# Performance work log

Measured on AMD Instinct MI355X. Metric: run time of the kernel, lower is better.

The kernel has to match this reference:

```python
import jax, jax.numpy as jnp
import numpy as np

BEAM = 10; MAX_LEN = 32; PAD = 1; BOS = 2; EOS = 3
NEG = jnp.float32(-1e30)


def lstm_cell(x, h, c, Wih, Whh, bih, bhh):
    # PyTorch LSTMCell gate order: i, f, g, o
    gates = x @ Wih.T + bih + h @ Whh.T + bhh
    i, f, g, o = jnp.split(gates, 4, axis=-1)
    c2 = jax.nn.sigmoid(f) * c + jax.nn.sigmoid(i) * jnp.tanh(g)
    h2 = jax.nn.sigmoid(o) * jnp.tanh(c2)
    return h2, c2


def setup_inputs() -> dict:
    key = jax.random.key(0)
    ks = jax.random.split(key, 14)
    G, P, E, H, S = 1000, 50000, 500, 500, 32
    s = lambda k, shape: jax.random.normal(k, shape, jnp.float32) * 0.05
    return {
        "g_seq": jax.random.randint(ks[0], (S, 1), 0, G),
        "enc_emb": s(ks[1], (G, E)),
        "enc_Wih": s(ks[2], (4 * H, E)), "enc_Whh": s(ks[3], (4 * H, H)),
        "enc_bih": s(ks[4], (4 * H,)), "enc_bhh": s(ks[5], (4 * H,)),
        "dec_emb": s(ks[6], (P, E)),
        "dec_Wih": s(ks[7], (4 * H, E)), "dec_Whh": s(ks[8], (4 * H, H)),
        "dec_bih": s(ks[9], (4 * H,)), "dec_bhh": s(ks[10], (4 * H,)),
        "attn_W": s(ks[11], (H, 2 * H)),
        "out_W": s(ks[12], (P, H)),
        "out_b": s(ks[13], (P,)),
    }


def reference(g_seq, enc_emb, enc_Wih, enc_Whh, enc_bih, enc_bhh,
              dec_emb, dec_Wih, dec_Whh, dec_bih, dec_bhh,
              attn_W, out_W, out_b):
    S = g_seq.shape[0]
    H = enc_Whh.shape[1]
    P = out_W.shape[0]

    # ---- encoder: unidirectional LSTMCell over seq, batch = 1 ----
    e_seq = enc_emb[g_seq[:, 0]]  # (S, E)
    def enc_step(carry, e):
        h, c = carry
        h, c = lstm_cell(e[None, :], h, c, enc_Wih, enc_Whh, enc_bih, enc_bhh)
        return (h, c), h[0]
    h0 = jnp.zeros((1, H), jnp.float32)
    (h, c), outs = jax.lax.scan(enc_step, (h0, h0), e_seq)  # outs: (S, H)

    # expand encoder state / context to beam
    context = jnp.broadcast_to(outs[None, :, :], (BEAM, S, H))
    h = jnp.broadcast_to(h, (BEAM, H))
    c = jnp.broadcast_to(c, (BEAM, H))
    scores = jnp.zeros((BEAM,), jnp.float32)
    tokens = jnp.full((BEAM,), PAD, jnp.int32).at[0].set(BOS)
    row0 = (jnp.arange(BEAM)[:, None] == 0)  # first-step mask: only beam 0 valid

    # ---- beam-search decode loop (run full max_len; early-eos break omitted,
    #      see notes: with eos=3 it only changes output when eos tops beam 0) ----
    def dec_step(carry, t):
        h, c, scores, tokens = carry
        e = dec_emb[tokens]                                   # (BEAM, E)
        h2, c2 = lstm_cell(e, h, c, dec_Wih, dec_Whh, dec_bih, dec_bhh)
        # dot attention
        attn = jax.nn.softmax(jnp.einsum('bsh,bh->bs', context, h2), axis=1)
        wctx = jnp.einsum('bs,bsh->bh', attn, context)
        o = jnp.tanh(jnp.concatenate([h2, wctx], axis=1) @ attn_W.T)
        logp = jax.nn.log_softmax(o @ out_W.T + out_b, axis=1)  # (BEAM, P)
        # first step: only beam 0 participates (original uses workd_lk[0])
        beam_lk = jnp.where(t == 0,
                            jnp.where(row0, logp, NEG),
                            logp + scores[:, None])
        best, idx = jax.lax.top_k(beam_lk.reshape(-1), BEAM)
        prev_k = idx // P
        next_y = idx - prev_k * P
        return (h2[prev_k], c2[prev_k], best, next_y), (prev_k, next_y)

    (_, _, scores, _), (prevKs, nextYs) = jax.lax.scan(
        dec_step, (h, c, scores, tokens), jnp.arange(MAX_LEN))

    # ---- hypothesis traceback, vectorized over beams ----
    def tb_step(k, t):
        tok = nextYs[t][k]
        return prevKs[t][k], tok
    _, toks = jax.lax.scan(tb_step, jnp.arange(BEAM), jnp.arange(MAX_LEN - 1, -1, -1))
    hyps = toks[::-1].T  # (BEAM, MAX_LEN)
    return hyps
```

## Files before the change

### kernel.cpp

```cpp
#include <hip/hip_runtime.h>
#include <hip/hip_cooperative_groups.h>
#include <math.h>

namespace cg = cooperative_groups;

#define BEAM   10
#define MAXLEN 32
#define SLEN   32
#define HD     500
#define ED     500
#define G4     2000
#define PV     50000
#define NEGF   (-1e30f)

#define GRID   256
#define NW     1024

#define NCHUNK 25
#define CHSZ   2000
#define CANDN  (NCHUNK * BEAM * BEAM)

#define OFF_X      0
#define OFF_CBUF   64000
#define OFF_GBUF   65000
#define OFF_CTX    69000
#define OFF_DH     85000
#define OFF_DC     90000
#define OFF_DG     95000
#define OFF_H2     115000
#define OFF_C2     120000
#define OFF_O      130000
#define OFF_SCD    135000
#define OFF_TOK    135020
#define OFF_PREVK  135040
#define OFF_NEXTY  135360
#define OFF_PARTD  136000
#define OFF_CAND   152000
#define OFF_LOG    160000
#define OFF_OWT    660000
#define NEED_T_BYTES ((size_t)(OFF_OWT + (size_t)HD * PV) * 4)

typedef unsigned long long u64;

__device__ __forceinline__ float sigf(float x) { return 1.f / (1.f + expf(-x)); }

__device__ __forceinline__ unsigned fkey(float f) {
    unsigned u = __float_as_uint(f);
    return (u & 0x80000000u) ? ~u : (u | 0x80000000u);
}
__device__ __forceinline__ float unfkey(unsigned k) {
    unsigned u = (k & 0x80000000u) ? (k & 0x7fffffffu) : ~k;
    return __uint_as_float(u);
}

__global__ void k_prep(const int* __restrict__ g_seq, const float* __restrict__ enc_emb,
                       const float* __restrict__ Wih, const float* __restrict__ bih,
                       const float* __restrict__ bhh, float* __restrict__ X,
                       float* __restrict__ cbuf0) {
    if (blockIdx.x == 0) {
        for (int j = threadIdx.x; j < HD; j += 256) cbuf0[j] = 0.f;
    }
    int wv = (blockIdx.x * blockDim.x + threadIdx.x) >> 6;
    int lane = threadIdx.x & 63;
    if (wv >= SLEN * G4) return;
    int t = wv / G4, r = wv - t * G4;
    const float* emb = enc_emb + (size_t)g_seq[t] * ED;
    const float* w = Wih + (size_t)r * ED;
    float acc = 0.f;
    for (int ki = 0; ki < 8; ki++) { int k = ki * 64 + lane; if (k < ED) acc += emb[k] * w[k]; }
    for (int o = 32; o; o >>= 1) acc += __shfl_down(acc, o);
    if (lane == 0) X[t * G4 + r] = acc + bih[r] + bhh[r];
}

__global__ void k_transpose4(const float* __restrict__ outW, float* __restrict__ outW4) {
    __shared__ float t_lds[64][65];
    int tid = threadIdx.x;
    int pbase = blockIdx.x * 64, kbase = blockIdx.y * 64;
    for (int e = 0; e < 16; e++) {
        int idx = e * 256 + tid; int pl = idx >> 6, kl = idx & 63;
        int pp = pbase + pl, kk = kbase + kl;
        t_lds[pl][kl] = (pp < PV && kk < HD) ? outW[(size_t)pp * HD + kk] : 0.f;
    }
    __syncthreads();
    for (int e = 0; e < 4; e++) {
        int idx = e * 256 + tid;
        int pl = idx & 63, kb = idx >> 6;
        int pp = pbase + pl;
        int kglob = kbase + kb * 4;
        if (pp < PV && kglob < HD) {
            float4 v;
            v.x = t_lds[pl][kb * 4 + 0];
            v.y = t_lds[pl][kb * 4 + 1];
            v.z = t_lds[pl][kb * 4 + 2];
            v.w = t_lds[pl][kb * 4 + 3];
            *(float4*)(outW4 + ((size_t)(kbase / 4 + kb) * PV + pp) * 4) = v;
        }
    }
}

struct MegaA {
    const float* encWhh; const float* X;
    float* gbuf; float* cbuf; float* ctx;
    const float* decEmb; const float* decWih; const float* decWhh;
    const float* decBih; const float* decBhh; const float* attnW;
    const float* outW4; const float* outW; const float* outB;
    float* dh; float* dc; float* dg; float* h2w; float* c2w; float* ow;
    float* logits; double* sc; double* part;
    int* tok; int* prevK; int* nextY; u64* cand; int* outTok;
    int bigws; int npart;
};

struct TopkSm { u64 wred[4]; u64 win; };
struct MergeSm {
    double wredd[4];
    double lse[BEAM];
    double scl[BEAM];
    double bwv[4];
    unsigned bwf[4];
    unsigned winf;
    int pk[BEAM]; int ny[BEAM];
    double val[BEAM];
};

__global__ __launch_bounds__(256) void k_mega(MegaA A) {
    __shared__ __align__(16) char smem_raw[43584];
    float* smf = (float*)smem_raw;
    cg::grid_group grid = cg::this_grid();
    const int tid = threadIdx.x, bid = blockIdx.x;
    const int wv = tid >> 6, lane = tid & 63;
    const int gw = bid * 4 + wv;

    for (int t = 0; t <= SLEN; ++t) {
        const float* gprev = A.gbuf + ((t + 1) & 1) * G4;
        float*       gcur  = A.gbuf + (t & 1) * G4;
        const float* cprev = A.cbuf + ((t + 1) & 1) * HD;
        float*       ccur  = A.cbuf + (t & 1) * HD;
        bool par = (t < SLEN) || (bid == 0);
        if (par) {
            float* h_lds = smf;
            if (t > 0) {
                for (int j = tid; j < HD; j += 256) {
                    float gi = gprev[j], gf = gprev[HD + j], gg = gprev[2 * HD + j], go = gprev[3 * HD + j];
                    float c = sigf(gf) * cprev[j] + sigf(gi) * tanhf(gg);
                    float h = sigf(go) * tanhf(c);
                    h_lds[j] = h;
                    if (bid == 0) {
                        ccur[j] = c;
                        A.ctx[(t - 1) * HD + j] = h;
                        if (t == SLEN) {
                            for (int b = 0; b < BEAM; b++) { A.dh[b * HD + j] = h; A.dc[b * HD + j] = c; }
                        }
                    }
                }
            } else {
                for (int j = tid; j < HD; j += 256) h_lds[j] = 0.f;
            }
            if (t == SLEN && bid == 0 && tid == 0) {
                for (int b = 0; b < BEAM; b++) A.sc[b] = 0.0;
                A.tok[0] = 2; for (int b = 1; b < BEAM; b++) A.tok[b] = 1;
            }
            __syncthreads();
            if (t < SLEN) {
                for (int r = gw; r < G4; r += NW) {
                    const float* w = A.encWhh + (size_t)r * HD;
                    float acc = 0.f;
                    for (int ki = 0; ki < 8; ki++) { int k = ki * 64 + lane; if (k < HD) acc += h_lds[k] * w[k]; }
                    for (int o = 32; o; o >>= 1) acc += __shfl_down(acc, o);
                    if (lane == 0) gcur[r] = A.X[t * G4 + r] + acc;
                }
            }
        }
        grid.sync();
    }

    for (int t = 0; t < MAXLEN; ++t) {
        {
            float* e_lds = smf;
            float* h_lds = smf + BEAM * ED;
            for (int idx = tid; idx < BEAM * ED; idx += 256) {
                int b = idx / ED, k = idx - b * ED;
                e_lds[idx] = A.decEmb[(size_t)A.tok[b] * ED + k];
                h_lds[idx] = A.dh[idx];
            }
            __syncthreads();
            for (int r = gw; r < G4; r += NW) {
                const float* wi = A.decWih + (size_t)r * ED;
                const float* wh = A.decWhh + (size_t)r * HD;
                float acc[BEAM];
#pragma unroll
                for (int b = 0; b < BEAM; b++) acc[b] = 0.f;
                for (int ki = 0; ki < 8; ki++) {
                    int k = ki * 64 + lane;
                    if (k < ED) {
                        float w = wi[k];
#pragma unroll
                        for (int b = 0; b < BEAM; b++) acc[b] += w * e_lds[b * ED + k];
                    }
                }
                for (int ki = 0; ki < 8; ki++) {
                    int k = ki * 64 + lane;
                    if (k < HD) {
                        float w = wh[k];
#pragma unroll
                        for (int b = 0; b < BEAM; b++) acc[b] += w * h_lds[b * HD + k];
                    }
                }
#pragma unroll
                for (int b = 0; b < BEAM; b++) {
                    float v = acc[b];
                    for (int o = 32; o; o >>= 1) v += __shfl_down(v, o);
                    acc[b] = v;
                }
                if (lane == 0) {
                    float bb = A.decBih[r] + A.decBhh[r];
#pragma unroll
                    for (int b = 0; b < BEAM; b++) A.dg[b * G4 + r] = acc[b] + bb;
                }
            }
        }
        grid.sync();

        if (bid < 125) {
            float* h2_lds   = smf;
            float* wctx_lds = smf + 5000;
            float* s_lds    = smf + 10000;
            float* a_lds    = smf + 10320;
            for (int idx = tid; idx < BEAM * HD; idx += 256) {
                int b = idx / HD, j = idx - b * HD;
                float gi = A.dg[b * G4 + j], gf = A.dg[b * G4 + HD + j];
                float gg = A.dg[b * G4 + 2 * HD + j], go = A.dg[b * G4 + 3 * HD + j];
                float c = sigf(gf) * A.dc[idx] + sigf(gi) * tanhf(gg);
                float h2 = sigf(go) * tanhf(c);
                h2_lds[idx] = h2;
                if (bid == 0) { A.c2w[idx] = c; A.h2w[idx] = h2; }
            }
            __syncthreads();
            for (int si = 0; si < 8; ++si) {
                int s = wv + 4 * si;
                float acc[BEAM];
#pragma unroll
                for (int b = 0; b < BEAM; b++) acc[b] = 0.f;
                for (int ki = 0; ki < 8; ki++) {
                    int k = ki * 64 + lane;
                    if (k < HD) {
                        float c = A.ctx[s * HD + k];
#pragma unroll
                        for (int b = 0; b < BEAM; b++) acc[b] += c * h2_lds[b * HD + k];
                    }
                }
#pragma unroll
                for (int b = 0; b < BEAM; b++) {
                    float v = acc[b];
                    for (int o = 32; o; o >>= 1) v += __shfl_down(v, o);
                    if (lane == 0) s_lds[b * SLEN + s] = v;
                }
            }
            __syncthreads();
            if (wv == 0) {
                for (int b = 0; b < BEAM; ++b) {
                    float v = (lane < SLEN) ? s_lds[b * SLEN + lane] : -INFINITY;
                    float m = v;
                    for (int o = 32; o; o >>= 1) m = fmaxf(m, __shfl_xor(m, o));
                    float e = (lane < SLEN) ? expf(v - m) : 0.f;
                    float sum = e;
                    for (int o = 32; o; o >>= 1) sum += __shfl_xor(sum, o);
                    if (lane < SLEN) a_lds[b * SLEN + lane] = e / sum;
                }
            }
            __syncthreads();
            {
                float w0[BEAM], w1[BEAM];
#pragma unroll
                for (int b = 0; b < BEAM; b++) { w0[b] = 0.f; w1[b] = 0.f; }
                int j0 = tid, j1 = tid + 256;
                for (int s = 0; s < SLEN; ++s) {
                    float c0 = (j0 < HD) ? A.ctx[s * HD + j0] : 0.f;
                    float c1 = (j1 < HD) ? A.ctx[s * HD + j1] : 0.f;
#pragma unroll
                    for (int b = 0; b < BEAM; b++) {
                        float a = a_lds[b * SLEN + s];
                        w0[b] += a * c0; w1[b] += a * c1;
                    }
                }
#pragma unroll
                for (int b = 0; b < BEAM; b++) {
                    if (j0 < HD) wctx_lds[b * HD + j0] = w0[b];
                    if (j1 < HD) wctx_lds[b * HD + j1] = w1[b];
                }
            }
            __syncthreads();
            int j = gw;
            const float* w = A.attnW + (size_t)j * 1000;
            float acc[BEAM];
#pragma unroll
            for (int b = 0; b < BEAM; b++) acc[b] = 0.f;
            for (int ki = 0; ki < 16; ki++) {
                int k = ki * 64 + lane;
                if (k < 1000) {
                    float wk = w[k];
#pragma unroll
                    for (int b = 0; b < BEAM; b++) {
                        float h = (k < HD) ? h2_lds[b * HD + k] : wctx_lds[b * HD + k - HD];
                        acc[b] += wk * h;
                    }
                }
            }
#pragma unroll
            for (int b = 0; b < BEAM; b++) {
                float v = acc[b];
                for (int o = 32; o; o >>= 1) v += __shfl_down(v, o);
                acc[b] = v;
            }
            if (lane == 0) {
#pragma unroll
                for (int b = 0; b < BEAM; b++) A.ow[b * HD + j] = tanhf(acc[b]);
            }
        }
        grid.sync();

        {
            float4* o4 = (float4*)smem_raw;
            for (int idx = tid; idx < BEAM * 125; idx += 256) {
                int b = idx / 125, kb = idx - b * 125;
                o4[idx] = *(const float4*)(A.ow + b * HD + kb * 4);
            }
            __syncthreads();
            if (A.bigws) {
                float* partl = (float*)(smem_raw + 20032);
                for (int pt = bid; pt < 782; pt += GRID) {
                    int kc = tid >> 6, pl = tid & 63;
                    int p = pt * 64 + pl;
                    int pc = (p < PV) ? p : (PV - 1);
                    int kb0 = kc * 32, kb1 = (kc == 3) ? 125 : (kb0 + 32);
                    float acc[BEAM];
#pragma unroll
                    for (int b = 0; b < BEAM; b++) acc[b] = 0.f;
                    const float4* wp = (const float4*)A.outW4;
                    for (int kb = kb0; kb < kb1; ++kb) {
                        float4 w = wp[(size_t)kb * PV + pc];
#pragma unroll
                        for (int b = 0; b < BEAM; b++) {
                            float4 o = o4[b * 125 + kb];
                            acc[b] += w.x * o.x + w.y * o.y + w.z * o.z + w.w * o.w;
                        }
                    }
#pragma unroll
                    for (int b = 0; b < BEAM; b++) partl[(kc * 64 + pl) * BEAM + b] = acc[b];
                    __syncthreads();
                    if (tid < 64) {
                        int p2 = pt * 64 + tid;
                        bool valid = (p2 < PV);
                        float ob = A.outB[valid ? p2 : 0];
                        double es[BEAM];
#pragma unroll
                        for (int b = 0; b < BEAM; b++) {
                            float lg = partl[(0 * 64 + tid) * BEAM + b] + partl[(1 * 64 + tid) * BEAM + b]
                                     + partl[(2 * 64 + tid) * BEAM + b] + partl[(3 * 64 + tid) * BEAM + b] + ob;
                            if (valid) A.logits[(size_t)b * PV + p2] = lg;
                            es[b] = valid ? exp((double)lg) : 0.0;
                        }
#pragma unroll
                        for (int b = 0; b < BEAM; b++) {
                            for (int o = 32; o; o >>= 1) es[b] += __shfl_down(es[b], o);
                        }
                        if (tid == 0) {
#pragma unroll
                            for (int b = 0; b < BEAM; b++) A.part[pt * BEAM + b] = es[b];
                        }
                    }
                    __syncthreads();
                }
            } else {
                float* o_lds = (float*)smem_raw;
                double* ered = (double*)(smem_raw + 20032);
                double esum = 0.0;
                for (int w = gw; w * 16 < PV; w += NW) {
                    for (int pi = 0; pi < 16; pi++) {
                        int p = w * 16 + pi;
                        if (p >= PV) break;
                        const float* wr = A.outW + (size_t)p * HD;
                        float acc[BEAM];
#pragma unroll
                        for (int b = 0; b < BEAM; b++) acc[b] = 0.f;
                        for (int ki = 0; ki < 8; ki++) {
                            int k = ki * 64 + lane;
                            if (k < HD) {
                                float x = wr[k];
#pragma unroll
                                for (int b = 0; b < BEAM; b++) acc[b] += x * o_lds[b * HD + k];
                            }
                        }
#pragma unroll
                        for (int b = 0; b < BEAM; b++)
                            for (int o = 32; o; o >>= 1) acc[b] += __shfl_xor(acc[b], o);
                        if (lane < BEAM) {
                            float lg = 0.f;
#pragma unroll
                            for (int b = 0; b < BEAM; b++) if (lane == b) lg = acc[b];
                            lg += A.outB[p];
                            A.logits[(size_t)lane * PV + p] = lg;
                            esum += exp((double)lg);
                        }
                    }
                }
                if (lane < BEAM) ered[wv * BEAM + lane] = esum;
                __syncthreads();
                if (tid < BEAM)
                    A.part[bid * BEAM + tid] = ered[0 * BEAM + tid] + ered[1 * BEAM + tid]
                                             + ered[2 * BEAM + tid] + ered[3 * BEAM + tid];
            }
        }
        grid.sync();

        if (bid < NCHUNK * BEAM) {
            TopkSm* T = (TopkSm*)smem_raw;
            int r = bid / NCHUNK, ci = bid - r * NCHUNK;
            int base = ci * CHSZ;
            u64 key[8];
#pragma unroll
            for (int e = 0; e < 8; e++) {
                int p = base + e * 256 + tid;
                key[e] = 0ull;
                if (p < base + CHSZ && p < PV) {
                    float v = A.logits[(size_t)r * PV + p];
                    key[e] = ((u64)fkey(v) << 32) | (unsigned)(~(unsigned)p);
                }
            }
            for (int round = 0; round < BEAM; round++) {
                u64 mx = 0ull;
#pragma unroll
                for (int e = 0; e < 8; e++) if (key[e] > mx) mx = key[e];
                for (int o = 32; o; o >>= 1) {
                    u64 other = __shfl_down(mx, o);
                    if (other > mx) mx = other;
                }
                if (lane == 0) T->wred[wv] = mx;
                __syncthreads();
                if (tid == 0) {
                    u64 wn = T->wred[0];
                    for (int i = 1; i < 4; i++) if (T->wred[i] > wn) wn = T->wred[i];
                    T->win = wn;
                    A.cand[bid * BEAM + round] = wn;
                }
                __syncthreads();
                u64 win = T->win;
#pragma unroll
                for (int e = 0; e < 8; e++) if (key[e] == win) key[e] = 0ull;
            }
        }
        grid.sync();

        if (bid == 0) {
            MergeSm* M = (MergeSm*)smem_raw;
            if (tid < BEAM) M->scl[tid] = A.sc[tid];
            for (int b = 0; b < BEAM; b++) {
                double s = 0.0;
                for (int j = tid; j < A.npart; j += 256) s += A.part[j * BEAM + b];
                for (int o = 32; o; o >>= 1) s += __shfl_down(s, o);
                if (lane == 0) M->wredd[wv] = s;
                __syncthreads();
                if (tid == 0) M->lse[b] = log(M->wredd[0] + M->wredd[1] + M->wredd[2] + M->wredd[3]);
                __syncthreads();
            }
            double   cv[10];
            unsigned cf[10];
#pragma unroll
            for (int e = 0; e < 10; e++) {
                int c = e * 256 + tid;
                cv[e] = -1.0e308; cf[e] = 0xFFFFFFFFu;
                if (c < CANDN) {
                    u64 k0 = A.cand[c];
                    if (k0) {
                        int r = c / (NCHUNK * BEAM);
                        float v = unfkey((unsigned)(k0 >> 32));
                        unsigned p = ~((unsigned)k0);
                        double v2;
                        if (t == 0) v2 = (r == 0) ? ((double)v - M->lse[0]) : (double)NEGF;
                        else        v2 = ((double)v - M->lse[r]) + M->scl[r];
                        cv[e] = v2;
                        cf[e] = (unsigned)r * PV + p;
                    }
                }
            }
            for (int round = 0; round < BEAM; round++) {
                double bv = -1.0e308; unsigned bf = 0xFFFFFFFFu;
#pragma unroll
                for (int e = 0; e < 10; e++) {
                    if (cv[e] > bv || (cv[e] == bv && cf[e] < bf)) { bv = cv[e]; bf = cf[e]; }
                }
                for (int o = 32; o; o >>= 1) {
                    double ov = __shfl_down(bv, o);
                    unsigned of = __shfl_down(bf, o);
                    if (ov > bv || (ov == bv && of < bf)) { bv = ov; bf = of; }
                }
                if (lane == 0) { M->bwv[wv] = bv; M->bwf[wv] = bf; }
                __syncthreads();
                if (tid == 0) {
                    double xv = M->bwv[0]; unsigned xf = M->bwf[0];
                    for (int i = 1; i < 4; i++) {
                        if (M->bwv[i] > xv || (M->bwv[i] == xv && M->bwf[i] < xf)) { xv = M->bwv[i]; xf = M->bwf[i]; }
                    }
                    M->winf = xf;
                    int pk = (int)(xf / PV);
                    int ny = (int)(xf - (unsigned)pk * PV);
                    M->pk[round] = pk; M->ny[round] = ny; M->val[round] = xv;
                }
                __syncthreads();
                unsigned wff = M->winf;
#pragma unroll
                for (int e = 0; e < 10; e++) {
                    if (cf[e] == wff) { cv[e] = -1.0e308; cf[e] = 0xFFFFFFFFu; }
                }
            }
            if (tid < BEAM) {
                A.sc[tid] = M->val[tid];
                A.tok[tid] = M->ny[tid];
                A.prevK[t * BEAM + tid] = M->pk[tid];
                A.nextY[t * BEAM + tid] = M->ny[tid];
            }
            __syncthreads();
            for (int idx = tid; idx < BEAM * HD; idx += 256) {
                int i = idx / HD, j = idx - i * HD;
                A.dh[idx] = A.h2w[M->pk[i] * HD + j];
                A.dc[idx] = A.c2w[M->pk[i] * HD + j];
            }
        }
        grid.sync();
    }

    if (bid == 0 && tid < BEAM) {
        int cur = tid;
        for (int tt = MAXLEN - 1; tt >= 0; tt--) {
            A.outTok[tid * MAXLEN + tt] = A.nextY[tt * BEAM + cur];
            cur = A.prevK[tt * BEAM + cur];
        }
    }
}

__global__ void k_enc(const float* __restrict__ Whh, const float* __restrict__ X,
                      float* __restrict__ gbuf, float* __restrict__ cbuf,
                      float* __restrict__ context, float* __restrict__ dec_h,
                      float* __restrict__ dec_c, double* __restrict__ scores,
                      int* __restrict__ tokens, int t) {
    __shared__ float h_lds[HD];
    const float* gprev = gbuf + ((t + 1) & 1) * G4;
    float*       gcur  = gbuf + (t & 1) * G4;
    const float* cprev = cbuf + ((t + 1) & 1) * HD;
    float*       ccur  = cbuf + (t & 1) * HD;
    int tid = threadIdx.x;
    if (t > 0) {
        for (int j = tid; j < HD; j += 256) {
            float gi = gprev[j], gf = gprev[HD + j], gg = gprev[2 * HD + j], go = gprev[3 * HD + j];
            float c = sigf(gf) * cprev[j] + sigf(gi) * tanhf(gg);
            float h = sigf(go) * tanhf(c);
            h_lds[j] = h;
            if (blockIdx.x == 0) {
                ccur[j] = c;
                context[(t - 1) * HD + j] = h;
                if (t == SLEN) {
                    for (int b = 0; b < BEAM; b++) { dec_h[b * HD + j] = h; dec_c[b * HD + j] = c; }
                }
            }
        }
    } else {
        for (int j = tid; j < HD; j += 256) h_lds[j] = 0.f;
    }
    if (t == SLEN && blockIdx.x == 0 && tid == 0) {
        for (int b = 0; b < BEAM; b++) scores[b] = 0.0;
        tokens[0] = 2; for (int b = 1; b < BEAM; b++) tokens[b] = 1;
    }
    __syncthreads();
    if (t < SLEN) {
        int wv = blockIdx.x * 4 + (tid >> 6), lane = tid & 63;
        for (int r = wv; r < G4; r += 1000) {
            const float* w = Whh + (size_t)r * HD;
            float acc = 0.f;
            for (int ki = 0; ki < 8; ki++) { int k = ki * 64 + lane; if (k < HD) acc += h_lds[k] * w[k]; }
            for (int o = 32; o; o >>= 1) acc += __shfl_down(acc, o);
            if (lane == 0) gcur[r] = X[t * G4 + r] + acc;
        }
    }
}

__global__ __launch_bounds__(1024) void k_gates(
        const float* __restrict__ dec_emb, const float* __restrict__ Wih,
        const float* __restrict__ Whh, const float* __restrict__ bih,
        const float* __restrict__ bhh, const int* __restrict__ tokens,
        const float* __restrict__ h_ws, float* __restrict__ gates) {
    __shared__ float e_lds[BEAM * ED];
    __shared__ float h_lds[BEAM * HD];
    int tid = threadIdx.x;
    for (int idx = tid; idx < BEAM * ED; idx += 1024) {
        int b = idx / ED, k = idx - b * ED;
        e_lds[idx] = dec_emb[(size_t)tokens[b] * ED + k];
        h_lds[idx] = h_ws[idx];
    }
    __syncthreads();
    int wv = tid >> 6, lane = tid & 63;
    int r = blockIdx.x * 16 + wv;
    const float* wi = Wih + (size_t)r * ED;
    const float* wh = Whh + (size_t)r * HD;
    float acc[BEAM];
#pragma unroll
    for (int b = 0; b < BEAM; b++) acc[b] = 0.f;
    for (int ki = 0; ki < 8; ki++) {
        int k = ki * 64 + lane;
        if (k < ED) {
            float w = wi[k];
#pragma unroll
            for (int b = 0; b < BEAM; b++) acc[b] += w * e_lds[b * ED + k];
        }
    }
    for (int ki = 0; ki < 8; ki++) {
        int k = ki * 64 + lane;
        if (k < HD) {
            float w = wh[k];
#pragma unroll
            for (int b = 0; b < BEAM; b++) acc[b] += w * h_lds[b * HD + k];
        }
    }
#pragma unroll
    for (int b = 0; b < BEAM; b++) {
        float v = acc[b];
        for (int o = 32; o; o >>= 1) v += __shfl_down(v, o);
        acc[b] = v;
    }
    if (lane == 0) {
        float bb = bih[r] + bhh[r];
#pragma unroll
        for (int b = 0; b < BEAM; b++) gates[b * G4 + r] = acc[b] + bb;
    }
}

__global__ __launch_bounds__(256) void k_attn_oproj(
        const float* __restrict__ gates, const float* __restrict__ c_ws,
        const float* __restrict__ context, const float* __restrict__ attnW,
        float* __restrict__ h2_ws, float* __restrict__ c2_ws, float* __restrict__ o_ws) {
    __shared__ float h2_lds[BEAM * HD];
    __shared__ float wctx_lds[BEAM * HD];
    __shared__ float s_lds[BEAM * SLEN];
    __shared__ float a_lds[BEAM * SLEN];
    int tid = threadIdx.x;
    int wv = tid >> 6, lane = tid & 63;
    for (int idx = tid; idx < BEAM * HD; idx += 256) {
        int b = idx / HD, j = idx - b * HD;
        float gi = gates[b * G4 + j], gf = gates[b * G4 + HD + j];
        float gg = gates[b * G4 + 2 * HD + j], go = gates[b * G4 + 3 * HD + j];
        float c = sigf(gf) * c_ws[idx] + sigf(gi) * tanhf(gg);
        float h2 = sigf(go) * tanhf(c);
        h2_lds[idx] = h2;
        if (blockIdx.x == 0) { c2_ws[idx] = c; h2_ws[idx] = h2; }
    }
    __syncthreads();
    for (int si = 0; si < 8; ++si) {
        int s = wv + 4 * si;
        float acc[BEAM];
#pragma unroll
        for (int b = 0; b < BEAM; b++) acc[b] = 0.f;
        for (int ki = 0; ki < 8; ki++) {
            int k = ki * 64 + lane;
            if (k < HD) {
                float c = context[s * HD + k];
#pragma unroll
                for (int b = 0; b < BEAM; b++) acc[b] += c * h2_lds[b * HD + k];
            }
        }
#pragma unroll
        for (int b = 0; b < BEAM; b++) {
            float v = acc[b];
            for (int o = 32; o; o >>= 1) v += __shfl_down(v, o);
            if (lane == 0) s_lds[b * SLEN + s] = v;
        }
    }
    __syncthreads();
    if (wv == 0) {
        for (int b = 0; b < BEAM; ++b) {
            float v = (lane < SLEN) ? s_lds[b * SLEN + lane] : -INFINITY;
            float m = v;
            for (int o = 32; o; o >>= 1) m = fmaxf(m, __shfl_xor(m, o));
            float e = (lane < SLEN) ? expf(v - m) : 0.f;
// ... 177 lines not shown
            if (other > mx) mx = other;
        }
        if (lane == 0) wred[wv] = mx;
        __syncthreads();
        if (tid == 0) {
            u64 wn = wred[0];
            for (int i = 1; i < 4; i++) if (wred[i] > wn) wn = wred[i];
            winlds = wn;
            cands[blockIdx.x * BEAM + round] = wn;
        }
        __syncthreads();
        u64 win = winlds;
#pragma unroll
        for (int e = 0; e < 7; e++) if (key[e] == win) key[e] = 0ull;
    }
}

__global__ __launch_bounds__(256) void k_merge(
        const double* __restrict__ partials, int npart,
        const u64* __restrict__ cands,
        double* __restrict__ scores, int* __restrict__ tokens,
        const float* __restrict__ h2_ws, const float* __restrict__ c2_ws,
        float* __restrict__ h_ws, float* __restrict__ c_ws,
        int* __restrict__ prevKs, int* __restrict__ nextYs, int t) {
    __shared__ double wredd[4];
    __shared__ double lse_lds[BEAM];
    __shared__ double sc_lds[BEAM];
    __shared__ double bwv[4];
    __shared__ unsigned bwf[4];
    __shared__ unsigned winf_s;
    __shared__ int pk_lds[BEAM];
    __shared__ int ny_lds[BEAM];
    __shared__ double val_lds[BEAM];
    int tid = threadIdx.x;
    int wv = tid >> 6, lane = tid & 63;
    if (tid < BEAM) sc_lds[tid] = scores[tid];
    for (int b = 0; b < BEAM; b++) {
        double s = 0.0;
        for (int j = tid; j < npart; j += 256) s += partials[j * BEAM + b];
        for (int o = 32; o; o >>= 1) s += __shfl_down(s, o);
        if (lane == 0) wredd[wv] = s;
        __syncthreads();
        if (tid == 0) lse_lds[b] = log(wredd[0] + wredd[1] + wredd[2] + wredd[3]);
        __syncthreads();
    }
    double   cv[13];
    unsigned cf[13];
#pragma unroll
    for (int e = 0; e < 13; e++) {
        int c = e * 256 + tid;
        cv[e] = -1.0e308; cf[e] = 0xFFFFFFFFu;
        if (c < 3200) {
            u64 k0 = cands[c];
            if (k0) {
                int r = c / 320;
                float v = unfkey((unsigned)(k0 >> 32));
                unsigned p = ~((unsigned)k0);
                double v2;
                if (t == 0) v2 = (r == 0) ? ((double)v - lse_lds[0]) : (double)NEGF;
                else        v2 = ((double)v - lse_lds[r]) + sc_lds[r];
                cv[e] = v2;
                cf[e] = (unsigned)r * PV + p;
            }
        }
    }
    for (int round = 0; round < BEAM; round++) {
        double bv = -1.0e308; unsigned bf = 0xFFFFFFFFu;
#pragma unroll
        for (int e = 0; e < 13; e++) {
            if (cv[e] > bv || (cv[e] == bv && cf[e] < bf)) { bv = cv[e]; bf = cf[e]; }
        }
        for (int o = 32; o; o >>= 1) {
            double ov = __shfl_down(bv, o);
            unsigned of = __shfl_down(bf, o);
            if (ov > bv || (ov == bv && of < bf)) { bv = ov; bf = of; }
        }
        if (lane == 0) { bwv[wv] = bv; bwf[wv] = bf; }
        __syncthreads();
        if (tid == 0) {
            double xv = bwv[0]; unsigned xf = bwf[0];
            for (int i = 1; i < 4; i++) {
                if (bwv[i] > xv || (bwv[i] == xv && bwf[i] < xf)) { xv = bwv[i]; xf = bwf[i]; }
            }
            winf_s = xf;
            int pk = (int)(xf / PV);
            int ny = (int)(xf - (unsigned)pk * PV);
            pk_lds[round] = pk; ny_lds[round] = ny; val_lds[round] = xv;
        }
        __syncthreads();
        unsigned wff = winf_s;
#pragma unroll
        for (int e = 0; e < 13; e++) {
            if (cf[e] == wff) { cv[e] = -1.0e308; cf[e] = 0xFFFFFFFFu; }
        }
    }
    if (tid < BEAM) {
        scores[tid] = val_lds[tid];
        tokens[tid] = ny_lds[tid];
        prevKs[t * BEAM + tid] = pk_lds[tid];
        nextYs[t * BEAM + tid] = ny_lds[tid];
    }
    __syncthreads();
    for (int idx = tid; idx < BEAM * HD; idx += 256) {
        int i = idx / HD, j = idx - i * HD;
        h_ws[idx] = h2_ws[pk_lds[i] * HD + j];
        c_ws[idx] = c2_ws[pk_lds[i] * HD + j];
    }
}

__global__ void k_traceback(const int* __restrict__ prevKs, const int* __restrict__ nextYs,
                            int* __restrict__ out) {
    int k = threadIdx.x;
    if (k >= BEAM) return;
    int cur = k;
    for (int t = MAXLEN - 1; t >= 0; t--) {
        out[k * MAXLEN + t] = nextYs[t * BEAM + cur];
        cur = prevKs[t * BEAM + cur];
    }
}

extern "C" void kernel_launch(void* const* d_in, const int* in_sizes, int n_in,
                              void* d_out, int out_size, void* d_ws, size_t ws_size,
                              hipStream_t stream) {
    const int*   g_seq  = (const int*)  d_in[0];
    const float* encEmb = (const float*)d_in[1];
    const float* encWih = (const float*)d_in[2];
    const float* encWhh = (const float*)d_in[3];
    const float* encBih = (const float*)d_in[4];
    const float* encBhh = (const float*)d_in[5];
    const float* decEmb = (const float*)d_in[6];
    const float* decWih = (const float*)d_in[7];
    const float* decWhh = (const float*)d_in[8];
    const float* decBih = (const float*)d_in[9];
    const float* decBhh = (const float*)d_in[10];
    const float* attnW  = (const float*)d_in[11];
    const float* outW   = (const float*)d_in[12];
    const float* outB   = (const float*)d_in[13];

    float* ws = (float*)d_ws;
    float*  X     = ws + OFF_X;
    float*  cbuf  = ws + OFF_CBUF;
    float*  gbuf  = ws + OFF_GBUF;
    float*  ctx   = ws + OFF_CTX;
    float*  dh    = ws + OFF_DH;
    float*  dc    = ws + OFF_DC;
    float*  dg    = ws + OFF_DG;
    float*  h2    = ws + OFF_H2;
    float*  c2    = ws + OFF_C2;
    float*  o     = ws + OFF_O;
    double* sc    = (double*)(ws + OFF_SCD);
    int*    tok   = (int*)(ws + OFF_TOK);
    int*    prevK = (int*)(ws + OFF_PREVK);
    int*    nextY = (int*)(ws + OFF_NEXTY);
    double* part  = (double*)(ws + OFF_PARTD);
    u64*    cand  = (u64*)(ws + OFF_CAND);
    float*  logits = ws + OFF_LOG;
    float*  outW4  = ws + OFF_OWT;

    bool bigws = (ws_size >= NEED_T_BYTES);

    k_prep<<<16000, 256, 0, stream>>>(g_seq, encEmb, encWih, encBih, encBhh, X, cbuf);
    if (bigws) k_transpose4<<<dim3(782, 8), 256, 0, stream>>>(outW, outW4);

    bool coop_ok = false;
    {
        int dev = 0;
        if (hipGetDevice(&dev) == hipSuccess) {
            hipDeviceProp_t prop;
            if (hipGetDeviceProperties(&prop, dev) == hipSuccess && prop.cooperativeLaunch) {
                int occ = 0;
                if (hipOccupancyMaxActiveBlocksPerMultiprocessor(&occ, (const void*)k_mega, 256, 0)
                        == hipSuccess) {
                    if ((long long)occ * prop.multiProcessorCount >= GRID) coop_ok = true;
                }
            }
        }
    }

    hipError_t err = hipErrorUnknown;
    if (coop_ok) {
        MegaA a;
        a.encWhh = encWhh; a.X = X;
        a.gbuf = gbuf; a.cbuf = cbuf; a.ctx = ctx;
        a.decEmb = decEmb; a.decWih = decWih; a.decWhh = decWhh;
        a.decBih = decBih; a.decBhh = decBhh; a.attnW = attnW;
        a.outW4 = outW4; a.outW = outW; a.outB = outB;
        a.dh = dh; a.dc = dc; a.dg = dg; a.h2w = h2; a.c2w = c2; a.ow = o;
        a.logits = logits; a.sc = sc; a.part = part;
        a.tok = tok; a.prevK = prevK; a.nextY = nextY; a.cand = cand;
        a.outTok = (int*)d_out;
        a.bigws = bigws ? 1 : 0;
        a.npart = bigws ? 782 : GRID;
        void* params[] = { (void*)&a };
        err = hipLaunchCooperativeKernel((const void*)k_mega, dim3(GRID), dim3(256),
                                         params, 0, stream);
    }
    if (err != hipSuccess) {
        for (int t = 0; t <= SLEN; t++)
            k_enc<<<250, 256, 0, stream>>>(encWhh, X, gbuf, cbuf, ctx, dh, dc, sc, tok, t);
        const int npart = 782;
        for (int t = 0; t < MAXLEN; t++) {
            k_gates<<<125, 1024, 0, stream>>>(decEmb, decWih, decWhh, decBih, decBhh, tok, dh, dg);
            k_attn_oproj<<<125, 256, 0, stream>>>(dg, dc, ctx, attnW, h2, c2, o);
            if (bigws) k_logits4<<<782, 256, 0, stream>>>(outW4, outB, o, logits, part);
            else       k_logits_f<<<782, 256, 0, stream>>>(outW, outB, o, logits, part);
            k_topk_row<<<320, 256, 0, stream>>>(logits, cand);
            k_merge<<<1, 256, 0, stream>>>(part, npart, cand, sc, tok, h2, c2, dh, dc, prevK, nextY, t);
        }
        k_traceback<<<1, 64, 0, stream>>>(prevK, nextY, (int*)d_out);
    }
}
```

Measured before the change: 4.217 ms.

## Fuse logits with per-strip top-k and replace cooperative grid sync with atomic barrier

```diff
diff --git a/kernel.cpp b/kernel.cpp
--- a/kernel.cpp
+++ b/kernel.cpp
@@ -1,8 +1,5 @@
 #include <hip/hip_runtime.h>
-#include <hip/hip_cooperative_groups.h>
 #include <math.h>
-
-namespace cg = cooperative_groups;
 
 #define BEAM   10
 #define MAXLEN 32
@@ -12,13 +9,13 @@
 #define G4     2000
 #define PV     50000
 #define NEGF   (-1e30f)
-
-#define GRID   256
+#define NEGD   (-1.0e30)
+
+#define GRID2  256
 #define NW     1024
-
-#define NCHUNK 25
-#define CHSZ   2000
-#define CANDN  (NCHUNK * BEAM * BEAM)
+#define STRIP  196
+
+typedef unsigned long long u64;
 
 #define OFF_X      0
 #define OFF_CBUF   64000
@@ -29,18 +26,21 @@
 #define OFF_DG     95000
 #define OFF_H2     115000
 #define OFF_C2     120000
-#define OFF_O      130000
+#define OFF_O      125000
 #define OFF_SCD    135000
 #define OFF_TOK    135020
 #define OFF_PREVK  135040
 #define OFF_NEXTY  135360
-#define OFF_PARTD  136000
-#define OFF_CAND   152000
+#define OFF_PARTF  136000
+#define OFF_CANDF  152000
 #define OFF_LOG    160000
+#define OFF_BAR    160000
+#define OFF_LSE    160008
+#define OFF_PARTD  160028
+#define OFF_RC     165148
+#define OFF_CAND   165348
 #define OFF_OWT    660000
 #define NEED_T_BYTES ((size_t)(OFF_OWT + (size_t)HD * PV) * 4)
-
-typedef unsigned long long u64;
 
 __device__ __forceinline__ float sigf(float x) { return 1.f / (1.f + expf(-x)); }
 
@@ -53,12 +53,29 @@
     return __uint_as_float(u);
 }
 
+__device__ __forceinline__ void gbar(int* cnt, int* gen) {
+    __syncthreads();
+    if (threadIdx.x == 0) {
+        int g = __hip_atomic_load(gen, __ATOMIC_RELAXED, __HIP_MEMORY_SCOPE_AGENT);
+        int a = __hip_atomic_fetch_add(cnt, 1, __ATOMIC_ACQ_REL, __HIP_MEMORY_SCOPE_AGENT);
+        if (a == GRID2 - 1) {
+            __hip_atomic_store(cnt, 0, __ATOMIC_RELAXED, __HIP_MEMORY_SCOPE_AGENT);
+            __hip_atomic_store(gen, g + 1, __ATOMIC_RELEASE, __HIP_MEMORY_SCOPE_AGENT);
+        } else {
+            while (__hip_atomic_load(gen, __ATOMIC_ACQUIRE, __HIP_MEMORY_SCOPE_AGENT) == g)
+                __builtin_amdgcn_s_sleep(16);
+        }
+    }
+    __syncthreads();
+}
+
 __global__ void k_prep(const int* __restrict__ g_seq, const float* __restrict__ enc_emb,
                        const float* __restrict__ Wih, const float* __restrict__ bih,
                        const float* __restrict__ bhh, float* __restrict__ X,
-                       float* __restrict__ cbuf0) {
+                       float* __restrict__ cbuf0, int* __restrict__ bar) {
     if (blockIdx.x == 0) {
         for (int j = threadIdx.x; j < HD; j += 256) cbuf0[j] = 0.f;
+        if (threadIdx.x < 8) bar[threadIdx.x] = 0;
     }
     int wv = (blockIdx.x * blockDim.x + threadIdx.x) >> 6;
     int lane = threadIdx.x & 63;
@@ -103,29 +120,23 @@
     float* gbuf; float* cbuf; float* ctx;
     const float* decEmb; const float* decWih; const float* decWhh;
     const float* decBih; const float* decBhh; const float* attnW;
-    const float* outW4; const float* outW; const float* outB;
+    const float* outW4; const float* outB;
     float* dh; float* dc; float* dg; float* h2w; float* c2w; float* ow;
-    float* logits; double* sc; double* part;
-    int* tok; int* prevK; int* nextY; u64* cand; int* outTok;
-    int bigws; int npart;
+    double* sc; double* part; double* lse;
+    int* tok; int* prevK; int* nextY; u64* cand; u64* rc; int* outTok;
+    int* bar;
 };
 
-struct TopkSm { u64 wred[4]; u64 win; };
-struct MergeSm {
-    double wredd[4];
-    double lse[BEAM];
-    double scl[BEAM];
-    double bwv[4];
-    unsigned bwf[4];
-    unsigned winf;
-    int pk[BEAM]; int ny[BEAM];
-    double val[BEAM];
+struct MS {
+    double scl[BEAM]; double lse2[BEAM];
+    double bwv[4]; unsigned bwf[4]; unsigned winf;
+    int pk[BEAM]; int ny[BEAM]; double val[BEAM];
 };
 
-__global__ __launch_bounds__(256) void k_mega(MegaA A) {
-    __shared__ __align__(16) char smem_raw[43584];
+__global__ __launch_bounds__(256) void k_mega2(MegaA A) {
+    __shared__ __align__(16) char smem_raw[44032];
     float* smf = (float*)smem_raw;
-    cg::grid_group grid = cg::this_grid();
+    int* cnt = A.bar, * gen = A.bar + 1, * done = A.bar + 2;
     const int tid = threadIdx.x, bid = blockIdx.x;
     const int wv = tid >> 6, lane = tid & 63;
     const int gw = bid * 4 + wv;
@@ -135,8 +146,7 @@
         float*       gcur  = A.gbuf + (t & 1) * G4;
         const float* cprev = A.cbuf + ((t + 1) & 1) * HD;
         float*       ccur  = A.cbuf + (t & 1) * HD;
-        bool par = (t < SLEN) || (bid == 0);
-        if (par) {
+        if (t < SLEN || bid == 0) {
             float* h_lds = smf;
             if (t > 0) {
                 for (int j = tid; j < HD; j += 256) {
@@ -170,13 +180,13 @@
                 }
             }
         }
-        grid.sync();
+        gbar(cnt, gen);
     }
 
     for (int t = 0; t < MAXLEN; ++t) {
         {
             float* e_lds = smf;
-            float* h_lds = smf + BEAM * ED;
+            float* h_lds = smf + 5000;
             for (int idx = tid; idx < BEAM * ED; idx += 256) {
                 int b = idx / ED, k = idx - b * ED;
                 e_lds[idx] = A.decEmb[(size_t)A.tok[b] * ED + k];
@@ -218,7 +228,7 @@
                 }
             }
         }
-        grid.sync();
+        gbar(cnt, gen);
 
         if (bid < 125) {
             float* h2_lds   = smf;
@@ -316,7 +326,7 @@
                 for (int b = 0; b < BEAM; b++) A.ow[b * HD + j] = tanhf(acc[b]);
             }
         }
-        grid.sync();
+        gbar(cnt, gen);
 
         {
             float4* o4 = (float4*)smem_raw;
@@ -325,207 +335,165 @@
                 o4[idx] = *(const float4*)(A.ow + b * HD + kb * 4);
             }
             __syncthreads();
-            if (A.bigws) {
-                float* partl = (float*)(smem_raw + 20032);
-                for (int pt = bid; pt < 782; pt += GRID) {
-                    int kc = tid >> 6, pl = tid & 63;
-                    int p = pt * 64 + pl;
-                    int pc = (p < PV) ? p : (PV - 1);
-                    int kb0 = kc * 32, kb1 = (kc == 3) ? 125 : (kb0 + 32);
-                    float acc[BEAM];
-#pragma unroll
-                    for (int b = 0; b < BEAM; b++) acc[b] = 0.f;
-                    const float4* wp = (const float4*)A.outW4;
-                    for (int kb = kb0; kb < kb1; ++kb) {
-                        float4 w = wp[(size_t)kb * PV + pc];
-#pragma unroll
-                        for (int b = 0; b < BEAM; b++) {
-                            float4 o = o4[b * 125 + kb];
-                            acc[b] += w.x * o.x + w.y * o.y + w.z * o.z + w.w * o.w;
-                        }
+            int p = bid * STRIP + tid;
+            bool valid = (tid < STRIP) && (p < PV);
+            int pc = (p < PV) ? p : (PV - 1);
+            float lg[BEAM];
+            {
+                float acc[BEAM];
+#pragma unroll
+                for (int b = 0; b < BEAM; b++) acc[b] = 0.f;
+                const float4* wp = (const float4*)A.outW4;
+                for (int kb = 0; kb < 125; ++kb) {
+                    float4 w = wp[(size_t)kb * PV + pc];
+#pragma unroll
+                    for (int b = 0; b < BEAM; b++) {
+                        float4 o = o4[b * 125 + kb];
+                        acc[b] += w.x * o.x + w.y * o.y + w.z * o.z + w.w * o.w;
                     }
-#pragma unroll
-                    for (int b = 0; b < BEAM; b++) partl[(kc * 64 + pl) * BEAM + b] = acc[b];
-                    __syncthreads();
-                    if (tid < 64) {
-                        int p2 = pt * 64 + tid;
-                        bool valid = (p2 < PV);
-                        float ob = A.outB[valid ? p2 : 0];
-                        double es[BEAM];
-#pragma unroll
-                        for (int b = 0; b < BEAM; b++) {
-                            float lg = partl[(0 * 64 + tid) * BEAM + b] + partl[(1 * 64 + tid) * BEAM + b]
-                                     + partl[(2 * 64 + tid) * BEAM + b] + partl[(3 * 64 + tid) * BEAM + b] + ob;
-                            if (valid) A.logits[(size_t)b * PV + p2] = lg;
-                            es[b] = valid ? exp((double)lg) : 0.0;
-                        }
-#pragma unroll
-                        for (int b = 0; b < BEAM; b++) {
-                            for (int o = 32; o; o >>= 1) es[b] += __shfl_down(es[b], o);
-                        }
-                        if (tid == 0) {
-#pragma unroll
-                            for (int b = 0; b < BEAM; b++) A.part[pt * BEAM + b] = es[b];
-                        }
+                }
+                float ob = A.outB[pc];
+#pragma unroll
+                for (int b = 0; b < BEAM; b++) lg[b] = acc[b] + ob;
+            }
+            double* pd = (double*)(smem_raw + 20480);
+#pragma unroll
+            for (int b = 0; b < BEAM; b++) pd[b * 256 + tid] = valid ? exp((double)lg[b]) : 0.0;
+            __syncthreads();
+            for (int r = wv; r < BEAM; r += 4) {
+                double s = pd[r * 256 + lane] + pd[r * 256 + 64 + lane]
+                         + pd[r * 256 + 128 + lane] + pd[r * 256 + 192 + lane];
+                for (int o = 32; o; o >>= 1) s += __shfl_down(s, o);
+                if (lane == 0) A.part[r * 256 + bid] = s;
+            }
+            __syncthreads();
+            u64* kl = (u64*)(smem_raw + 20480);
+#pragma unroll
+            for (int b = 0; b < BEAM; b++)
+                kl[b * 256 + tid] = valid ? (((u64)fkey(lg[b]) << 32) | (unsigned)(~(unsigned)p)) : 0ull;
+            __syncthreads();
+            for (int r = wv; r < BEAM; r += 4) {
+                u64 kk[4];
+#pragma unroll
+                for (int j = 0; j < 4; j++) kk[j] = kl[r * 256 + j * 64 + lane];
+                for (int round = 0; round < BEAM; round++) {
+                    u64 m = kk[0];
+                    if (kk[1] > m) m = kk[1];
+                    if (kk[2] > m) m = kk[2];
+                    if (kk[3] > m) m = kk[3];
+                    for (int o = 32; o; o >>= 1) {
+                        u64 t2 = __shfl_down(m, o);
+                        if (t2 > m) m = t2;
                     }
-                    __syncthreads();
-                }
-            } else {
-                float* o_lds = (float*)smem_raw;
-                double* ered = (double*)(smem_raw + 20032);
-                double esum = 0.0;
-                for (int w = gw; w * 16 < PV; w += NW) {
-                    for (int pi = 0; pi < 16; pi++) {
-                        int p = w * 16 + pi;
-                        if (p >= PV) break;
-                        const float* wr = A.outW + (size_t)p * HD;
-                        float acc[BEAM];
-#pragma unroll
-                        for (int b = 0; b < BEAM; b++) acc[b] = 0.f;
-                        for (int ki = 0; ki < 8; ki++) {
-                            int k = ki * 64 + lane;
-                            if (k < HD) {
-                                float x = wr[k];
-#pragma unroll
-                                for (int b = 0; b < BEAM; b++) acc[b] += x * o_lds[b * HD + k];
-                            }
-                        }
-#pragma unroll
-                        for (int b = 0; b < BEAM; b++)
-                            for (int o = 32; o; o >>= 1) acc[b] += __shfl_xor(acc[b], o);
-                        if (lane < BEAM) {
-                            float lg = 0.f;
-#pragma unroll
-                            for (int b = 0; b < BEAM; b++) if (lane == b) lg = acc[b];
-                            lg += A.outB[p];
-                            A.logits[(size_t)lane * PV + p] = lg;
-                            esum += exp((double)lg);
-                        }
-                    }
-                }
-                if (lane < BEAM) ered[wv * BEAM + lane] = esum;
+                    u64 win = __shfl(m, 0);
+#pragma unroll
+                    for (int j = 0; j < 4; j++) if (kk[j] == win) kk[j] = 0ull;
+                    if (lane == 0) A.cand[(size_t)r * 2560 + bid * 10 + round] = win;
+                }
+            }
+        }
+        gbar(cnt, gen);
+
+        if (bid < BEAM) {
+            int r = bid;
+            double* redd = (double*)(smem_raw + 40960);
+            u64* wred = (u64*)(smem_raw + 41024);
+            u64* winp = (u64*)(smem_raw + 41056);
+            int* lastf = (int*)(smem_raw + 41072);
+            {
+                double s = A.part[r * 256 + tid];
+                for (int o = 32; o; o >>= 1) s += __shfl_down(s, o);
+                if (lane == 0) redd[wv] = s;
                 __syncthreads();
-                if (tid < BEAM)
-                    A.part[bid * BEAM + tid] = ered[0 * BEAM + tid] + ered[1 * BEAM + tid]
-                                             + ered[2 * BEAM + tid] + ered[3 * BEAM + tid];
-            }
-        }
-        grid.sync();
-
-        if (bid < NCHUNK * BEAM) {
-            TopkSm* T = (TopkSm*)smem_raw;
-            int r = bid / NCHUNK, ci = bid - r * NCHUNK;
-            int base = ci * CHSZ;
-            u64 key[8];
-#pragma unroll
-            for (int e = 0; e < 8; e++) {
-                int p = base + e * 256 + tid;
-                key[e] = 0ull;
-                if (p < base + CHSZ && p < PV) {
-                    float v = A.logits[(size_t)r * PV + p];
-                    key[e] = ((u64)fkey(v) << 32) | (unsigned)(~(unsigned)p);
-                }
-            }
+                if (tid == 0) A.lse[r] = log(redd[0] + redd[1] + redd[2] + redd[3]);
+            }
+            u64 kk[10];
+#pragma unroll
+            for (int e = 0; e < 10; e++) kk[e] = A.cand[(size_t)r * 2560 + e * 256 + tid];
             for (int round = 0; round < BEAM; round++) {
-                u64 mx = 0ull;
-#pragma unroll
-                for (int e = 0; e < 8; e++) if (key[e] > mx) mx = key[e];
+                u64 m = 0ull;
+#pragma unroll
+                for (int e = 0; e < 10; e++) if (kk[e] > m) m = kk[e];
                 for (int o = 32; o; o >>= 1) {
-                    u64 other = __shfl_down(mx, o);
-                    if (other > mx) mx = other;
-                }
-                if (lane == 0) T->wred[wv] = mx;
+                    u64 t2 = __shfl_down(m, o);
+                    if (t2 > m) m = t2;
+                }
+                if (lane == 0) wred[wv] = m;
                 __syncthreads();
                 if (tid == 0) {
-                    u64 wn = T->wred[0];
-                    for (int i = 1; i < 4; i++) if (T->wred[i] > wn) wn = T->wred[i];
-                    T->win = wn;
-                    A.cand[bid * BEAM + round] = wn;
+                    u64 wn = wred[0];
+                    for (int i = 1; i < 4; i++) if (wred[i] > wn) wn = wred[i];
+                    *winp = wn;
+                    A.rc[r * 10 + round] = wn;
                 }
                 __syncthreads();
-                u64 win = T->win;
-#pragma unroll
-                for (int e = 0; e < 8; e++) if (key[e] == win) key[e] = 0ull;
-            }
-        }
-        grid.sync();
-
-        if (bid == 0) {
-            MergeSm* M = (MergeSm*)smem_raw;
-            if (tid < BEAM) M->scl[tid] = A.sc[tid];
-            for (int b = 0; b < BEAM; b++) {
-                double s = 0.0;
-                for (int j = tid; j < A.npart; j += 256) s += A.part[j * BEAM + b];
-                for (int o = 32; o; o >>= 1) s += __shfl_down(s, o);
-                if (lane == 0) M->wredd[wv] = s;
+                u64 win = *winp;
+#pragma unroll
+                for (int e = 0; e < 10; e++) if (kk[e] == win) kk[e] = 0ull;
                 __syncthreads();
-                if (tid == 0) M->lse[b] = log(M->wredd[0] + M->wredd[1] + M->wredd[2] + M->wredd[3]);
+            }
+            if (tid == 0) {
+                int old = __hip_atomic_fetch_add(done, 1, __ATOMIC_ACQ_REL, __HIP_MEMORY_SCOPE_AGENT);
+                *lastf = (old == BEAM - 1) ? 1 : 0;
+            }
+            __syncthreads();
+            if (*lastf) {
+                MS* M = (MS*)(smem_raw + 41216);
+                if (tid < BEAM) { M->scl[tid] = A.sc[tid]; M->lse2[tid] = A.lse[tid]; }
                 __syncthreads();
-            }
-            double   cv[10];
-            unsigned cf[10];
-#pragma unroll
-            for (int e = 0; e < 10; e++) {
-                int c = e * 256 + tid;
-                cv[e] = -1.0e308; cf[e] = 0xFFFFFFFFu;
-                if (c < CANDN) {
-                    u64 k0 = A.cand[c];
+                double cv = -1.0e308; unsigned cf = 0xFFFFFFFFu;
+                if (tid < BEAM * BEAM) {
+                    u64 k0 = A.rc[tid];
                     if (k0) {
-                        int r = c / (NCHUNK * BEAM);
+                        int r2 = tid / BEAM;
                         float v = unfkey((unsigned)(k0 >> 32));
                         unsigned p = ~((unsigned)k0);
                         double v2;
-                        if (t == 0) v2 = (r == 0) ? ((double)v - M->lse[0]) : (double)NEGF;
-                        else        v2 = ((double)v - M->lse[r]) + M->scl[r];
-                        cv[e] = v2;
-                        cf[e] = (unsigned)r * PV + p;
+                        if (t == 0) v2 = (r2 == 0) ? ((double)v - M->lse2[0]) : NEGD;
+                        else        v2 = ((double)v - M->lse2[r2]) + M->scl[r2];
+                        cv = v2;
+                        cf = (unsigned)r2 * PV + p;
                     }
                 }
-            }
-            for (int round = 0; round < BEAM; round++) {
-                double bv = -1.0e308; unsigned bf = 0xFFFFFFFFu;
-#pragma unroll
-                for (int e = 0; e < 10; e++) {
-                    if (cv[e] > bv || (cv[e] == bv && cf[e] < bf)) { bv = cv[e]; bf = cf[e]; }
-                }
-                for (int o = 32; o; o >>= 1) {
-                    double ov = __shfl_down(bv, o);
-                    unsigned of = __shfl_down(bf, o);
-                    if (ov > bv || (ov == bv && of < bf)) { bv = ov; bf = of; }
-                }
-                if (lane == 0) { M->bwv[wv] = bv; M->bwf[wv] = bf; }
+                for (int round = 0; round < BEAM; round++) {
+                    double bv = cv; unsigned bf = cf;
+                    for (int o = 32; o; o >>= 1) {
+                        double ov = __shfl_down(bv, o);
+                        unsigned of = __shfl_down(bf, o);
+                        if (ov > bv || (ov == bv && of < bf)) { bv = ov; bf = of; }
+                    }
+                    if (lane == 0) { M->bwv[wv] = bv; M->bwf[wv] = bf; }
+                    __syncthreads();
+                    if (tid == 0) {
+                        double xv = M->bwv[0]; unsigned xf = M->bwf[0];
+                        for (int i = 1; i < 4; i++) {
+                            if (M->bwv[i] > xv || (M->bwv[i] == xv && M->bwf[i] < xf)) { xv = M->bwv[i]; xf = M->bwf[i]; }
+                        }
+                        M->winf = xf;
+                        int pk = (int)(xf / PV);
+                        int ny = (int)(xf - (unsigned)pk * PV);
+                        M->pk[round] = pk; M->ny[round] = ny; M->val[round] = xv;
+                    }
+                    __syncthreads();
+                    if (cf == M->winf) { cv = -1.0e308; cf = 0xFFFFFFFFu; }
+                    __syncthreads();
+                }
+                if (tid < BEAM) {
+                    A.sc[tid] = M->val[tid];
+                    A.tok[tid] = M->ny[tid];
+                    A.prevK[t * BEAM + tid] = M->pk[tid];
+                    A.nextY[t * BEAM + tid] = M->ny[tid];
+                }
                 __syncthreads();
-                if (tid == 0) {
-                    double xv = M->bwv[0]; unsigned xf = M->bwf[0];
-                    for (int i = 1; i < 4; i++) {
-                        if (M->bwv[i] > xv || (M->bwv[i] == xv && M->bwf[i] < xf)) { xv = M->bwv[i]; xf = M->bwf[i]; }
-                    }
-                    M->winf = xf;
-                    int pk = (int)(xf / PV);
-                    int ny = (int)(xf - (unsigned)pk * PV);
-                    M->pk[round] = pk; M->ny[round] = ny; M->val[round] = xv;
-                }
-                __syncthreads();
-                unsigned wff = M->winf;
-#pragma unroll
-                for (int e = 0; e < 10; e++) {
-                    if (cf[e] == wff) { cv[e] = -1.0e308; cf[e] = 0xFFFFFFFFu; }
-                }
-            }
-            if (tid < BEAM) {
-                A.sc[tid] = M->val[tid];
-                A.tok[tid] = M->ny[tid];
-                A.prevK[t * BEAM + tid] = M->pk[tid];
-                A.nextY[t * BEAM + tid] = M->ny[tid];
-            }
-            __syncthreads();
-            for (int idx = tid; idx < BEAM * HD; idx += 256) {
-                int i = idx / HD, j = idx - i * HD;
-                A.dh[idx] = A.h2w[M->pk[i] * HD + j];
-                A.dc[idx] = A.c2w[M->pk[i] * HD + j];
-            }
-        }
-        grid.sync();
+                for (int idx = tid; idx < BEAM * HD; idx += 256) {
+                    int i = idx / HD, j = idx - i * HD;
+                    A.dh[idx] = A.h2w[M->pk[i] * HD + j];
+                    A.dc[idx] = A.c2w[M->pk[i] * HD + j];
+                }
+                if (tid == 0) __hip_atomic_store(done, 0, __ATOMIC_RELAXED, __HIP_MEMORY_SCOPE_AGENT);
+            }
+        }
+        gbar(cnt, gen);
     }
 
     if (bid == 0 && tid < BEAM) {
@@ -1009,50 +977,44 @@
     int*    tok   = (int*)(ws + OFF_TOK);
     int*    prevK = (int*)(ws + OFF_PREVK);
     int*    nextY = (int*)(ws + OFF_NEXTY);
-    double* part  = (double*)(ws + OFF_PARTD);
-    u64*    cand  = (u64*)(ws + OFF_CAND);
-    float*  logits = ws + OFF_LOG;
-    float*  outW4  = ws + OFF_OWT;
+    int*    bar   = (int*)(ws + OFF_BAR);
+    float*  outW4 = ws + OFF_OWT;
 
     bool bigws = (ws_size >= NEED_T_BYTES);
 
-    k_prep<<<16000, 256, 0, stream>>>(g_seq, encEmb, encWih, encBih, encBhh, X, cbuf);
+    k_prep<<<16000, 256, 0, stream>>>(g_seq, encEmb, encWih, encBih, encBhh, X, cbuf, bar);
     if (bigws) k_transpose4<<<dim3(782, 8), 256, 0, stream>>>(outW, outW4);
 
-    bool coop_ok = false;
-    {
+    bool mega_ok = bigws;
+    if (mega_ok) {
         int dev = 0;
-        if (hipGetDevice(&dev) == hipSuccess) {
-            hipDeviceProp_t prop;
-            if (hipGetDeviceProperties(&prop, dev) == hipSuccess && prop.cooperativeLaunch) {
-                int occ = 0;
-                if (hipOccupancyMaxActiveBlocksPerMultiprocessor(&occ, (const void*)k_mega, 256, 0)
-                        == hipSuccess) {
-                    if ((long long)occ * prop.multiProcessorCount >= GRID) coop_ok = true;
-                }
-            }
-        }
-    }
-
-    hipError_t err = hipErrorUnknown;
-    if (coop_ok) {
+        hipDeviceProp_t prop;
+        int occ = 0;
+        if (hipGetDevice(&dev) != hipSuccess ||
+            hipGetDeviceProperties(&prop, dev) != hipSuccess ||
+            hipOccupancyMaxActiveBlocksPerMultiprocessor(&occ, (const void*)k_mega2, 256, 0) != hipSuccess ||
+            (long long)occ * prop.multiProcessorCount < GRID2) {
+            mega_ok = false;
+        }
+    }
+
+    if (mega_ok) {
         MegaA a;
         a.encWhh = encWhh; a.X = X;
         a.gbuf = gbuf; a.cbuf = cbuf; a.ctx = ctx;
         a.decEmb = decEmb; a.decWih = decWih; a.decWhh = decWhh;
         a.decBih = decBih; a.decBhh = decBhh; a.attnW = attnW;
-        a.outW4 = outW4; a.outW = outW; a.outB = outB;
+        a.outW4 = outW4; a.outB = outB;
         a.dh = dh; a.dc = dc; a.dg = dg; a.h2w = h2; a.c2w = c2; a.ow = o;
-        a.logits = logits; a.sc = sc; a.part = part;
-        a.tok = tok; a.prevK = prevK; a.nextY = nextY; a.cand = cand;
-        a.outTok = (int*)d_out;
-        a.bigws = bigws ? 1 : 0;
-        a.npart = bigws ? 782 : GRID;
-        void* params[] = { (void*)&a };
-        err = hipLaunchCooperativeKernel((const void*)k_mega, dim3(GRID), dim3(256),
-                                         params, 0, stream);
-    }
-    if (err != hipSuccess) {
+        a.sc = sc; a.part = (double*)(ws + OFF_PARTD); a.lse = (double*)(ws + OFF_LSE);
+        a.tok = tok; a.prevK = prevK; a.nextY = nextY;
+        a.cand = (u64*)(ws + OFF_CAND); a.rc = (u64*)(ws + OFF_RC);
+        a.outTok = (int*)d_out; a.bar = bar;
+        k_mega2<<<GRID2, 256, 0, stream>>>(a);
+    } else {
+        double* part  = (double*)(ws + OFF_PARTF);
+        u64*    cand  = (u64*)(ws + OFF_CANDF);
+        float*  logits = ws + OFF_LOG;
         for (int t = 0; t <= SLEN; t++)
             k_enc<<<250, 256, 0, stream>>>(encWhh, X, gbuf, cbuf, ctx, dh, dc, sc, tok, t);
         const int npart = 782;
```

Measured after the change: 4.216 ms. No clear change (-0.0%).
